# Kernel optimization log

Measured on AMD Instinct MI355X. Metric: run time of the kernel, lower is better.

Reference implementation:

```python
import jax, jax.numpy as jnp
import numpy as np

N_NODES = 50000
N_EDGES = 800000
D_IN = 256
D_OUT = 256


def setup_inputs() -> dict:
    key = jax.random.key(0)
    ks = jax.random.split(key, 8)
    x = jax.random.normal(ks[0], (N_NODES, D_IN), dtype=jnp.float32)
    edge_index = jax.random.randint(ks[1], (2, N_EDGES), 0, N_NODES, dtype=jnp.int64)
    W_src = jax.random.normal(ks[2], (D_IN, D_OUT), dtype=jnp.float32) * 0.05
    b_src = jax.random.normal(ks[3], (D_OUT,), dtype=jnp.float32) * 0.05
    W_dst = jax.random.normal(ks[4], (D_IN, D_OUT), dtype=jnp.float32) * 0.05
    b_dst = jax.random.normal(ks[5], (D_OUT,), dtype=jnp.float32) * 0.05
    W_self = jax.random.normal(ks[6], (D_IN, D_OUT), dtype=jnp.float32) * 0.05
    b_self = jax.random.normal(ks[7], (D_OUT,), dtype=jnp.float32) * 0.05
    return {"x": x, "edge_index": edge_index, "W_src": W_src, "b_src": b_src,
            "W_dst": W_dst, "b_dst": b_dst, "W_self": W_self, "b_self": b_self}


def reference(x, edge_index, W_src, b_src, W_dst, b_dst, W_self, b_self):
    # LEConv: messages = src_linear(x[row]) - dst_linear(x[col]);
    # scatter-add messages into destination nodes (col); add self_linear(x).
    # Linear commutes with row-gather, so project once on [N, d] then gather.
    row, col = edge_index[0], edge_index[1]
    src = x @ W_src + b_src            # [N, D_OUT]
    dst = x @ W_dst + b_dst            # [N, D_OUT]
    messages = src[row] - dst[col]     # [E, D_OUT]
    agg = jax.ops.segment_sum(messages, col, num_segments=x.shape[0])  # [N, D_OUT]
    return x @ W_self + b_self + agg
```

## Files before the change

kernel.cpp:

```cpp
#include <hip/hip_runtime.h>

#define D 256

typedef unsigned short ushort_t;
typedef unsigned int uint_t;
typedef __attribute__((ext_vector_type(8))) short short8;
typedef __attribute__((ext_vector_type(4))) float floatx4;

static __device__ __forceinline__ ushort_t f2bf(float f) {
    union { float f; uint_t u; } c; c.f = f;
    uint_t r = (c.u + 0x7FFFu + ((c.u >> 16) & 1u)) >> 16;
    return (ushort_t)r;
}
static __device__ __forceinline__ float bf2f(ushort_t b) {
    union { uint_t u; float f; } c; c.u = ((uint_t)b) << 16;
    return c.f;
}

__global__ void prep_kernel(const int* __restrict__ col, int* __restrict__ deg,
                            const float* __restrict__ x, ushort_t* __restrict__ xh,
                            const float* __restrict__ Wself, const float* __restrict__ Wsrc,
                            const float* __restrict__ Wdst, ushort_t* __restrict__ BT,
                            int E, int total8, int degB, int cvtB) {
    int b = blockIdx.x;
    if (b < degB) {
        int e = b * 256 + threadIdx.x;
        if (e < E) atomicAdd(&deg[col[e]], 1);
    } else if (b < degB + cvtB) {
        int i = (b - degB) * 256 + threadIdx.x;
        if (i >= total8) return;
        float4 a = ((const float4*)x)[i * 2];
        float4 bb = ((const float4*)x)[i * 2 + 1];
        uint4 o;
        o.x = f2bf(a.x) | ((uint_t)f2bf(a.y) << 16);
        o.y = f2bf(a.z) | ((uint_t)f2bf(a.w) << 16);
        o.z = f2bf(bb.x) | ((uint_t)f2bf(bb.y) << 16);
        o.w = f2bf(bb.z) | ((uint_t)f2bf(bb.w) << 16);
        ((uint4*)xh)[i] = o;
    } else {
        int id = (b - degB - cvtB) * 256 + threadIdx.x;
        if (id >= 256 * 768) return;
        int j = id / 768, k = id % 768;
        float v;
        if (k < 256)      v = Wself[(size_t)k * 256 + j];
        else if (k < 512) v = Wsrc [(size_t)(k - 256) * 256 + j];
        else              v = Wdst [(size_t)(k - 512) * 256 + j];
        BT[id] = f2bf(v);
    }
}

__global__ __launch_bounds__(1024) void scan_kernel(const int* __restrict__ deg,
                                                    int* __restrict__ off,
                                                    int* __restrict__ cursor, int n4) {
    __shared__ int wsum[16];
    __shared__ int chunk_total;
    __shared__ int carry_s;
    const int tid = threadIdx.x, lane = tid & 63, wid = tid >> 6;
    if (tid == 0) carry_s = 0;
    __syncthreads();
    for (int base4 = 0; base4 < n4; base4 += 1024) {
        int i4 = base4 + tid;
        int4 v = (i4 < n4) ? ((const int4*)deg)[i4] : make_int4(0, 0, 0, 0);
        int s = v.x + v.y + v.z + v.w;
        int incl = s;
        #pragma unroll
        for (int st = 1; st < 64; st <<= 1) {
            int t = __shfl_up(incl, st, 64);
            if (lane >= st) incl += t;
        }
        if (lane == 63) wsum[wid] = incl;
        __syncthreads();
        if (wid == 0) {
            int wv = (lane < 16) ? wsum[lane] : 0;
            int wincl = wv;
            #pragma unroll
            for (int st = 1; st < 16; st <<= 1) {
                int t = __shfl_up(wincl, st, 64);
                if (lane >= st) wincl += t;
            }
            if (lane < 16) wsum[lane] = wincl - wv;
            if (lane == 15) chunk_total = wincl;
        }
        __syncthreads();
        int excl = incl - s + wsum[wid] + carry_s;
        if (i4 < n4) {
            int4 o;
            o.x = excl; o.y = o.x + v.x; o.z = o.y + v.y; o.w = o.z + v.z;
            ((int4*)off)[i4] = o;
            ((int4*)cursor)[i4] = o;
        }
        __syncthreads();
        if (tid == 0) carry_s += chunk_total;
        __syncthreads();
    }
}

__global__ void bucket_kernel(const int* __restrict__ row, const int* __restrict__ col,
                              int* __restrict__ cursor, int* __restrict__ bucket, int E) {
    int e = blockIdx.x * blockDim.x + threadIdx.x;
    if (e >= E) return;
    int pos = atomicAdd(&cursor[col[e]], 1);
    bucket[pos] = row[e];
}

__global__ __launch_bounds__(256) void segsum_kernel(const ushort_t* __restrict__ xh,
                                                     const int* __restrict__ off,
                                                     const int* __restrict__ deg,
                                                     const int* __restrict__ bucket,
                                                     ushort_t* __restrict__ Gh, int N) {
    int node = blockIdx.x * 4 + (threadIdx.x >> 6);
    int lane = threadIdx.x & 63;
    if (node >= N) return;
    int start = off[node];
    int cnt = deg[node];
    float a0 = 0.f, a1 = 0.f, a2 = 0.f, a3 = 0.f;
    int i = 0;
    for (; i + 2 <= cnt; i += 2) {
        int r0 = bucket[start + i];
        int r1 = bucket[start + i + 1];
        ushort4 v0 = ((const ushort4*)(xh + (size_t)r0 * D))[lane];
        ushort4 v1 = ((const ushort4*)(xh + (size_t)r1 * D))[lane];
        a0 += bf2f(v0.x) + bf2f(v1.x);
        a1 += bf2f(v0.y) + bf2f(v1.y);
        a2 += bf2f(v0.z) + bf2f(v1.z);
        a3 += bf2f(v0.w) + bf2f(v1.w);
    }
    if (i < cnt) {
        int r0 = bucket[start + i];
        ushort4 v0 = ((const ushort4*)(xh + (size_t)r0 * D))[lane];
        a0 += bf2f(v0.x); a1 += bf2f(v0.y); a2 += bf2f(v0.z); a3 += bf2f(v0.w);
    }
    ushort4 o;
    o.x = f2bf(a0); o.y = f2bf(a1); o.z = f2bf(a2); o.w = f2bf(a3);
    ((ushort4*)(Gh + (size_t)node * D))[lane] = o;
}

__global__ __launch_bounds__(256, 2) void mfma_gemm(
    const ushort_t* __restrict__ xh, const ushort_t* __restrict__ Gh,
    const ushort_t* __restrict__ BT, const int* __restrict__ deg,
    const float* __restrict__ bsrc, const float* __restrict__ bdst,
    const float* __restrict__ bself, float* __restrict__ out, int N)
{
    __shared__ ushort_t As[128][40];
    __shared__ ushort_t Bs[128][40];
    __shared__ ushort_t Ds[128][40];

    const int tid = threadIdx.x;
    const int lane = tid & 63, wave = tid >> 6;
    const int quad = lane >> 4, l15 = lane & 15;
    const int m0 = (wave >> 1) * 64, n0 = (wave & 1) * 64;
    const int mbase = blockIdx.x * 128, nbase = blockIdx.y * 128;

    floatx4 acc1[4][4] = {};
    floatx4 acc2[4][4] = {};

    for (int kt = 0; kt < 16; ++kt) {
        const int kcol = (kt & 7) * 32;
        const ushort_t* Asrc = (kt < 8) ? xh : Gh;

        #pragma unroll
        for (int h = 0; h < 2; ++h) {
            int c = tid + h * 256;
            int row = c >> 2, cc = c & 3;
            int gr = mbase + row; if (gr >= N) gr = N - 1;
            uint4 v = *(const uint4*)(Asrc + (size_t)gr * 256 + kcol + cc * 8);
            *(uint4*)(&As[row][cc * 8]) = v;
            int gn = nbase + row;
            uint4 w = *(const uint4*)(BT + (size_t)gn * 768 + kt * 32 + cc * 8);
            *(uint4*)(&Bs[row][cc * 8]) = w;
            if (kt < 8) {
                uint4 d = *(const uint4*)(BT + (size_t)gn * 768 + 512 + kt * 32 + cc * 8);
                *(uint4*)(&Ds[row][cc * 8]) = d;
            }
        }
        __syncthreads();

        short8 af[4], bfr[4];
        #pragma unroll
        for (int im = 0; im < 4; ++im)
            af[im] = *(const short8*)(&As[m0 + im * 16 + l15][quad * 8]);
        #pragma unroll
        for (int in = 0; in < 4; ++in)
            bfr[in] = *(const short8*)(&Bs[n0 + in * 16 + l15][quad * 8]);
        #pragma unroll
        for (int im = 0; im < 4; ++im)
            #pragma unroll
            for (int in = 0; in < 4; ++in)
                acc1[im][in] = __builtin_amdgcn_mfma_f32_16x16x32_bf16(
                    af[im], bfr[in], acc1[im][in], 0, 0, 0);
        if (kt < 8) {
            short8 df[4];
            #pragma unroll
            for (int in = 0; in < 4; ++in)
                df[in] = *(const short8*)(&Ds[n0 + in * 16 + l15][quad * 8]);
            #pragma unroll
            for (int im = 0; im < 4; ++im)
                #pragma unroll
                for (int in = 0; in < 4; ++in)
                    acc2[im][in] = __builtin_amdgcn_mfma_f32_16x16x32_bf16(
                        af[im], df[in], acc2[im][in], 0, 0, 0);
        }
        __syncthreads();
    }

    float degv[4][4];
    #pragma unroll
    for (int im = 0; im < 4; ++im)
        #pragma unroll
        for (int r = 0; r < 4; ++r) {
            int gm = mbase + m0 + im * 16 + quad * 4 + r;
            degv[im][r] = (gm < N) ? (float)deg[gm] : 0.f;
        }

    #pragma unroll
    for (int in = 0; in < 4; ++in) {
        int gn = nbase + n0 + in * 16 + l15;
        float bs = bself[gn];
        float db = bsrc[gn] - bdst[gn];
        #pragma unroll
        for (int im = 0; im < 4; ++im) {
            #pragma unroll
            for (int r = 0; r < 4; ++r) {
                int gm = mbase + m0 + im * 16 + quad * 4 + r;
                if (gm < N) {
                    float d = degv[im][r];
                    out[(size_t)gm * 256 + gn] =
                        acc1[im][in][r] - d * acc2[im][in][r] + bs + d * db;
                }
            }
        }
    }
}

extern "C" void kernel_launch(void* const* d_in, const int* in_sizes, int n_in,
                              void* d_out, int out_size, void* d_ws, size_t ws_size,
                              hipStream_t stream) {
    const float* x     = (const float*)d_in[0];
    const int*   eidx  = (const int*)d_in[1];
    const float* Wsrc  = (const float*)d_in[2];
    const float* bsrc  = (const float*)d_in[3];
    const float* Wdst  = (const float*)d_in[4];
    const float* bdst  = (const float*)d_in[5];
    const float* Wself = (const float*)d_in[6];
    const float* bself = (const float*)d_in[7];
    float* out = (float*)d_out;

    const int N = in_sizes[0] / D;
    const int E = in_sizes[1] / 2;
    const int* row = eidx;
    const int* col = eidx + E;

    char* p = (char*)d_ws;
    ushort_t* xh  = (ushort_t*)p;        p += (size_t)N * D * sizeof(ushort_t);
    ushort_t* Gh  = (ushort_t*)p;        p += (size_t)N * D * sizeof(ushort_t);
    ushort_t* BT  = (ushort_t*)p;        p += (size_t)768 * 256 * sizeof(ushort_t);
    int* deg      = (int*)p;             p += (size_t)N * sizeof(int);
    int* off      = (int*)p;             p += (size_t)N * sizeof(int);
    int* cursor   = (int*)p;             p += (size_t)N * sizeof(int);
    int* bucket   = (int*)p;

    hipMemsetAsync(deg, 0, (size_t)N * sizeof(int), stream);

    const int total8 = N * D / 8;
    const int degB = (E + 255) / 256;
    const int cvtB = (total8 + 255) / 256;
    const int btB  = (256 * 768 + 255) / 256;
    prep_kernel<<<degB + cvtB + btB, 256, 0, stream>>>(col, deg, x, xh,
                                                       Wself, Wsrc, Wdst, BT,
                                                       E, total8, degB, cvtB);
    scan_kernel<<<1, 1024, 0, stream>>>(deg, off, cursor, N / 4);
    bucket_kernel<<<(E + 255) / 256, 256, 0, stream>>>(row, col, cursor, bucket, E);
    segsum_kernel<<<(N + 3) / 4, 256, 0, stream>>>(xh, off, deg, bucket, Gh, N);

    dim3 grid((N + 127) / 128, 2);
    mfma_gemm<<<grid, 256, 0, stream>>>(xh, Gh, BT, deg, bsrc, bdst, bself, out, N);
}
```

Before: 317.7 us.

## Use atomic ranks for CSR fill, parallel scan, async LDS loads in GEMM

The degree-count pass now records each edge's atomic rank, so the bucket fill needs no second atomic pass. The single-block serial scan becomes a two-kernel multi-block scan. The segment-sum loop is unrolled to four gathers, and the GEMM stages tiles through global_load_lds direct-to-LDS loads with a fragment-ordered LDS layout. Together these aim to cut atomic contention, serial scan latency and register-staged tile copies, at the cost of more kernel launches and reusing the Gh buffer to hold rank.

Result: faster. 281.9 us (-11.3%).

```diff
diff --git a/kernel.cpp b/kernel.cpp
--- a/kernel.cpp
+++ b/kernel.cpp
@@ -17,7 +17,14 @@
     return c.f;
 }
 
+static __device__ __forceinline__ void async16(const void* g, void* l) {
+    __builtin_amdgcn_global_load_lds(
+        (const __attribute__((address_space(1))) void*)g,
+        (__attribute__((address_space(3))) void*)l, 16, 0, 0);
+}
+
 __global__ void prep_kernel(const int* __restrict__ col, int* __restrict__ deg,
+                            int* __restrict__ rank,
                             const float* __restrict__ x, ushort_t* __restrict__ xh,
                             const float* __restrict__ Wself, const float* __restrict__ Wsrc,
                             const float* __restrict__ Wdst, ushort_t* __restrict__ BT,
@@ -25,7 +32,7 @@
     int b = blockIdx.x;
     if (b < degB) {
         int e = b * 256 + threadIdx.x;
-        if (e < E) atomicAdd(&deg[col[e]], 1);
+        if (e < E) rank[e] = atomicAdd(&deg[col[e]], 1);
     } else if (b < degB + cvtB) {
         int i = (b - degB) * 256 + threadIdx.x;
         if (i >= total8) return;
@@ -49,58 +56,60 @@
     }
 }
 
-__global__ __launch_bounds__(1024) void scan_kernel(const int* __restrict__ deg,
-                                                    int* __restrict__ off,
-                                                    int* __restrict__ cursor, int n4) {
-    __shared__ int wsum[16];
-    __shared__ int chunk_total;
-    __shared__ int carry_s;
+__global__ __launch_bounds__(256) void scanA(const int* __restrict__ deg,
+                                             int* __restrict__ off,
+                                             int* __restrict__ partials, int n4) {
+    __shared__ int wtot[4];
     const int tid = threadIdx.x, lane = tid & 63, wid = tid >> 6;
-    if (tid == 0) carry_s = 0;
+    int i4 = blockIdx.x * 256 + tid;
+    int4 v = (i4 < n4) ? ((const int4*)deg)[i4] : make_int4(0, 0, 0, 0);
+    int s = v.x + v.y + v.z + v.w;
+    int incl = s;
+    #pragma unroll
+    for (int st = 1; st < 64; st <<= 1) {
+        int t = __shfl_up(incl, st, 64);
+        if (lane >= st) incl += t;
+    }
+    if (lane == 63) wtot[wid] = incl;
     __syncthreads();
-    for (int base4 = 0; base4 < n4; base4 += 1024) {
-        int i4 = base4 + tid;
-        int4 v = (i4 < n4) ? ((const int4*)deg)[i4] : make_int4(0, 0, 0, 0);
-        int s = v.x + v.y + v.z + v.w;
-        int incl = s;
-        #pragma unroll
-        for (int st = 1; st < 64; st <<= 1) {
-            int t = __shfl_up(incl, st, 64);
-            if (lane >= st) incl += t;
-        }
-        if (lane == 63) wsum[wid] = incl;
-        __syncthreads();
-        if (wid == 0) {
-            int wv = (lane < 16) ? wsum[lane] : 0;
-            int wincl = wv;
-            #pragma unroll
-            for (int st = 1; st < 16; st <<= 1) {
-                int t = __shfl_up(wincl, st, 64);
-                if (lane >= st) wincl += t;
-            }
-            if (lane < 16) wsum[lane] = wincl - wv;
-            if (lane == 15) chunk_total = wincl;
-        }
-        __syncthreads();
-        int excl = incl - s + wsum[wid] + carry_s;
-        if (i4 < n4) {
-            int4 o;
-            o.x = excl; o.y = o.x + v.x; o.z = o.y + v.y; o.w = o.z + v.z;
-            ((int4*)off)[i4] = o;
-            ((int4*)cursor)[i4] = o;
-        }
-        __syncthreads();
-        if (tid == 0) carry_s += chunk_total;
-        __syncthreads();
-    }
-}
-
-__global__ void bucket_kernel(const int* __restrict__ row, const int* __restrict__ col,
-                              int* __restrict__ cursor, int* __restrict__ bucket, int E) {
+    int wbase = 0;
+    #pragma unroll
+    for (int w = 0; w < 4; ++w) if (w < wid) wbase += wtot[w];
+    int excl = incl - s + wbase;
+    if (i4 < n4) {
+        int4 o;
+        o.x = excl; o.y = o.x + v.x; o.z = o.y + v.y; o.w = o.z + v.z;
+        ((int4*)off)[i4] = o;
+    }
+    if (tid == 0) partials[blockIdx.x] = wtot[0] + wtot[1] + wtot[2] + wtot[3];
+}
+
+__global__ __launch_bounds__(256) void scanC(int* __restrict__ off,
+                                             const int* __restrict__ partials, int n4) {
+    __shared__ int base_s;
+    const int tid = threadIdx.x;
+    if (tid < 64) {
+        int v = (tid < blockIdx.x) ? partials[tid] : 0;
+        #pragma unroll
+        for (int st = 32; st; st >>= 1) v += __shfl_down(v, st, 64);
+        if (tid == 0) base_s = v;
+    }
+    __syncthreads();
+    int base = base_s;
+    int i4 = blockIdx.x * 256 + tid;
+    if (i4 < n4) {
+        int4 o = ((int4*)off)[i4];
+        o.x += base; o.y += base; o.z += base; o.w += base;
+        ((int4*)off)[i4] = o;
+    }
+}
+
+__global__ void fill_kernel(const int* __restrict__ row, const int* __restrict__ col,
+                            const int* __restrict__ rank, const int* __restrict__ off,
+                            int* __restrict__ bucket, int E) {
     int e = blockIdx.x * blockDim.x + threadIdx.x;
     if (e >= E) return;
-    int pos = atomicAdd(&cursor[col[e]], 1);
-    bucket[pos] = row[e];
+    bucket[off[col[e]] + rank[e]] = row[e];
 }
 
 __global__ __launch_bounds__(256) void segsum_kernel(const ushort_t* __restrict__ xh,
@@ -115,17 +124,21 @@
     int cnt = deg[node];
     float a0 = 0.f, a1 = 0.f, a2 = 0.f, a3 = 0.f;
     int i = 0;
-    for (; i + 2 <= cnt; i += 2) {
+    for (; i + 4 <= cnt; i += 4) {
         int r0 = bucket[start + i];
         int r1 = bucket[start + i + 1];
+        int r2 = bucket[start + i + 2];
+        int r3 = bucket[start + i + 3];
         ushort4 v0 = ((const ushort4*)(xh + (size_t)r0 * D))[lane];
         ushort4 v1 = ((const ushort4*)(xh + (size_t)r1 * D))[lane];
-        a0 += bf2f(v0.x) + bf2f(v1.x);
-        a1 += bf2f(v0.y) + bf2f(v1.y);
-        a2 += bf2f(v0.z) + bf2f(v1.z);
-        a3 += bf2f(v0.w) + bf2f(v1.w);
-    }
-    if (i < cnt) {
+        ushort4 v2 = ((const ushort4*)(xh + (size_t)r2 * D))[lane];
+        ushort4 v3 = ((const ushort4*)(xh + (size_t)r3 * D))[lane];
+        a0 += (bf2f(v0.x) + bf2f(v1.x)) + (bf2f(v2.x) + bf2f(v3.x));
+        a1 += (bf2f(v0.y) + bf2f(v1.y)) + (bf2f(v2.y) + bf2f(v3.y));
+        a2 += (bf2f(v0.z) + bf2f(v1.z)) + (bf2f(v2.z) + bf2f(v3.z));
+        a3 += (bf2f(v0.w) + bf2f(v1.w)) + (bf2f(v2.w) + bf2f(v3.w));
+    }
+    for (; i < cnt; ++i) {
         int r0 = bucket[start + i];
         ushort4 v0 = ((const ushort4*)(xh + (size_t)r0 * D))[lane];
         a0 += bf2f(v0.x); a1 += bf2f(v0.y); a2 += bf2f(v0.z); a3 += bf2f(v0.w);
@@ -141,47 +154,48 @@
     const float* __restrict__ bsrc, const float* __restrict__ bdst,
     const float* __restrict__ bself, float* __restrict__ out, int N)
 {
-    __shared__ ushort_t As[128][40];
-    __shared__ ushort_t Bs[128][40];
-    __shared__ ushort_t Ds[128][40];
+    __shared__ ushort_t As[8][64][8];
+    __shared__ ushort_t Bs[8][64][8];
+    __shared__ ushort_t Ds[8][64][8];
 
     const int tid = threadIdx.x;
     const int lane = tid & 63, wave = tid >> 6;
     const int quad = lane >> 4, l15 = lane & 15;
-    const int m0 = (wave >> 1) * 64, n0 = (wave & 1) * 64;
+    const int mg = (wave >> 1) * 4, ng = (wave & 1) * 4;
     const int mbase = blockIdx.x * 128, nbase = blockIdx.y * 128;
+
+    const int ga0 = wave * 2, ga1 = ga0 + 1;
+    int ar0 = mbase + ga0 * 16 + l15; if (ar0 >= N) ar0 = N - 1;
+    int ar1 = mbase + ga1 * 16 + l15; if (ar1 >= N) ar1 = N - 1;
+    const size_t aoff0 = (size_t)ar0 * 256 + quad * 8;
+    const size_t aoff1 = (size_t)ar1 * 256 + quad * 8;
+    const ushort_t* bp0 = BT + (size_t)(nbase + ga0 * 16 + l15) * 768 + quad * 8;
+    const ushort_t* bp1 = BT + (size_t)(nbase + ga1 * 16 + l15) * 768 + quad * 8;
 
     floatx4 acc1[4][4] = {};
     floatx4 acc2[4][4] = {};
 
     for (int kt = 0; kt < 16; ++kt) {
-        const int kcol = (kt & 7) * 32;
         const ushort_t* Asrc = (kt < 8) ? xh : Gh;
-
-        #pragma unroll
-        for (int h = 0; h < 2; ++h) {
-            int c = tid + h * 256;
-            int row = c >> 2, cc = c & 3;
-            int gr = mbase + row; if (gr >= N) gr = N - 1;
-            uint4 v = *(const uint4*)(Asrc + (size_t)gr * 256 + kcol + cc * 8);
-            *(uint4*)(&As[row][cc * 8]) = v;
-            int gn = nbase + row;
-            uint4 w = *(const uint4*)(BT + (size_t)gn * 768 + kt * 32 + cc * 8);
-            *(uint4*)(&Bs[row][cc * 8]) = w;
-            if (kt < 8) {
-                uint4 d = *(const uint4*)(BT + (size_t)gn * 768 + 512 + kt * 32 + cc * 8);
-                *(uint4*)(&Ds[row][cc * 8]) = d;
-            }
+        const int ka = (kt & 7) * 32;
+        const int kb = kt * 32;
+        async16(Asrc + aoff0 + ka, &As[ga0][0][0]);
+        async16(Asrc + aoff1 + ka, &As[ga1][0][0]);
+        async16(bp0 + kb, &Bs[ga0][0][0]);
+        async16(bp1 + kb, &Bs[ga1][0][0]);
+        if (kt < 8) {
+            async16(bp0 + 512 + kb, &Ds[ga0][0][0]);
+            async16(bp1 + 512 + kb, &Ds[ga1][0][0]);
         }
         __syncthreads();
 
         short8 af[4], bfr[4];
         #pragma unroll
         for (int im = 0; im < 4; ++im)
-            af[im] = *(const short8*)(&As[m0 + im * 16 + l15][quad * 8]);
+            af[im] = *(const short8*)(&As[mg + im][lane][0]);
         #pragma unroll
         for (int in = 0; in < 4; ++in)
-            bfr[in] = *(const short8*)(&Bs[n0 + in * 16 + l15][quad * 8]);
+            bfr[in] = *(const short8*)(&Bs[ng + in][lane][0]);
         #pragma unroll
         for (int im = 0; im < 4; ++im)
             #pragma unroll
@@ -192,7 +206,7 @@
             short8 df[4];
             #pragma unroll
             for (int in = 0; in < 4; ++in)
-                df[in] = *(const short8*)(&Ds[n0 + in * 16 + l15][quad * 8]);
+                df[in] = *(const short8*)(&Ds[ng + in][lane][0]);
             #pragma unroll
             for (int im = 0; im < 4; ++im)
                 #pragma unroll
@@ -208,20 +222,20 @@
     for (int im = 0; im < 4; ++im)
         #pragma unroll
         for (int r = 0; r < 4; ++r) {
-            int gm = mbase + m0 + im * 16 + quad * 4 + r;
+            int gm = mbase + (wave >> 1) * 64 + im * 16 + quad * 4 + r;
             degv[im][r] = (gm < N) ? (float)deg[gm] : 0.f;
         }
 
     #pragma unroll
     for (int in = 0; in < 4; ++in) {
-        int gn = nbase + n0 + in * 16 + l15;
+        int gn = nbase + (wave & 1) * 64 + in * 16 + l15;
         float bs = bself[gn];
         float db = bsrc[gn] - bdst[gn];
         #pragma unroll
         for (int im = 0; im < 4; ++im) {
             #pragma unroll
             for (int r = 0; r < 4; ++r) {
-                int gm = mbase + m0 + im * 16 + quad * 4 + r;
+                int gm = mbase + (wave >> 1) * 64 + im * 16 + quad * 4 + r;
                 if (gm < N) {
                     float d = degv[im][r];
                     out[(size_t)gm * 256 + gn] =
@@ -252,11 +266,12 @@
 
     char* p = (char*)d_ws;
     ushort_t* xh  = (ushort_t*)p;        p += (size_t)N * D * sizeof(ushort_t);
-    ushort_t* Gh  = (ushort_t*)p;        p += (size_t)N * D * sizeof(ushort_t);
+    ushort_t* Gh  = (ushort_t*)p;        int* rank = (int*)p;
+                                         p += (size_t)N * D * sizeof(ushort_t);
     ushort_t* BT  = (ushort_t*)p;        p += (size_t)768 * 256 * sizeof(ushort_t);
     int* deg      = (int*)p;             p += (size_t)N * sizeof(int);
     int* off      = (int*)p;             p += (size_t)N * sizeof(int);
-    int* cursor   = (int*)p;             p += (size_t)N * sizeof(int);
+    int* partials = (int*)p;             p += 64 * sizeof(int);
     int* bucket   = (int*)p;
 
     hipMemsetAsync(deg, 0, (size_t)N * sizeof(int), stream);
@@ -265,11 +280,14 @@
     const int degB = (E + 255) / 256;
     const int cvtB = (total8 + 255) / 256;
     const int btB  = (256 * 768 + 255) / 256;
-    prep_kernel<<<degB + cvtB + btB, 256, 0, stream>>>(col, deg, x, xh,
+    prep_kernel<<<degB + cvtB + btB, 256, 0, stream>>>(col, deg, rank, x, xh,
                                                        Wself, Wsrc, Wdst, BT,
                                                        E, total8, degB, cvtB);
-    scan_kernel<<<1, 1024, 0, stream>>>(deg, off, cursor, N / 4);
-    bucket_kernel<<<(E + 255) / 256, 256, 0, stream>>>(row, col, cursor, bucket, E);
+    const int n4 = N / 4;
+    const int nblk = (n4 + 255) / 256;
+    scanA<<<nblk, 256, 0, stream>>>(deg, off, partials, n4);
+    scanC<<<nblk, 256, 0, stream>>>(off, partials, n4);
+    fill_kernel<<<(E + 255) / 256, 256, 0, stream>>>(row, col, rank, off, bucket, E);
     segsum_kernel<<<(N + 3) / 4, 256, 0, stream>>>(xh, off, deg, bucket, Gh, N);
 
     dim3 grid((N + 127) / 128, 2);
```
